# Kernel tuning notes

Measured on AMD Instinct MI355X. Metric: run time of the kernel, lower is better.

Reference implementation:

```python
import jax, jax.numpy as jnp
import numpy as np

N = 50000      # nodes
E = 800000     # edges (avg degree 16)
F_IN = 128     # num_features
H1 = 256       # hidden_dims[0]
H2 = 128       # hidden_dims[1]
D_EMB = 64     # embedding_dim
C_CLS = 2      # num_classes
EPS = 1e-5     # BatchNorm eps


def setup_inputs() -> dict:
    key = jax.random.key(0)
    ks = jax.random.split(key, 24)
    f32 = jnp.float32
    def w(k, shape, scale=0.05):
        return jax.random.normal(k, shape, f32) * scale
    inp = {
        "x": jax.random.normal(ks[0], (N, F_IN), f32),
        "edge_index": jax.random.randint(ks[1], (2, E), 0, N, jnp.int32),
        # input_proj
        "Wp": w(ks[2], (F_IN, H1)), "bp": jnp.zeros((H1,), f32),
        # conv1 (SAGEConv): lin_l (neighbors, with bias), lin_r (root, no bias)
        "W1l": w(ks[3], (F_IN, H1)), "b1l": jnp.zeros((H1,), f32), "W1r": w(ks[4], (F_IN, H1)),
        # bn1 (eval mode, running stats)
        "bn1_g": jnp.ones((H1,), f32), "bn1_b": jnp.zeros((H1,), f32),
        "bn1_m": w(ks[5], (H1,), 0.01), "bn1_v": jnp.ones((H1,), f32) + 0.1 * jax.random.uniform(ks[6], (H1,), f32),
        # skip_proj
        "Wsk": w(ks[7], (H1, H2)), "bsk": jnp.zeros((H2,), f32),
        # conv2
        "W2l": w(ks[8], (H1, H2)), "b2l": jnp.zeros((H2,), f32), "W2r": w(ks[9], (H1, H2)),
        # bn2
        "bn2_g": jnp.ones((H2,), f32), "bn2_b": jnp.zeros((H2,), f32),
        "bn2_m": w(ks[10], (H2,), 0.01), "bn2_v": jnp.ones((H2,), f32) + 0.1 * jax.random.uniform(ks[11], (H2,), f32),
        # conv3
        "W3l": w(ks[12], (H2, D_EMB)), "b3l": jnp.zeros((D_EMB,), f32), "W3r": w(ks[13], (H2, D_EMB)),
        # classifier
        "Wc": w(ks[14], (D_EMB, C_CLS)), "bc": jnp.zeros((C_CLS,), f32),
    }
    return inp


def _sage(h, src, dst, Wl, bl, Wr):
    # mean aggregation of source features into destination nodes
    s = jax.ops.segment_sum(h[src], dst, num_segments=N)        # [N, d]
    cnt = jax.ops.segment_sum(jnp.ones((src.shape[0], 1), h.dtype), dst, num_segments=N)
    mean = s / jnp.maximum(cnt, 1.0)
    return mean @ Wl + bl + h @ Wr


def _bn(h, g, b, m, v):
    return (h - m) * jax.lax.rsqrt(v + EPS) * g + b


def reference(x, edge_index, Wp, bp, W1l, b1l, W1r, bn1_g, bn1_b, bn1_m, bn1_v,
              Wsk, bsk, W2l, b2l, W2r, bn2_g, bn2_b, bn2_m, bn2_v,
              W3l, b3l, W3r, Wc, bc):
    src, dst = edge_index[0], edge_index[1]
    identity = x @ Wp + bp                                # input_proj
    h = _sage(x, src, dst, W1l, b1l, W1r)                 # conv1
    h = jax.nn.relu(_bn(h, bn1_g, bn1_b, bn1_m, bn1_v) + identity)
    # dropout is identity in eval mode
    identity = h @ Wsk + bsk                              # skip_proj
    h = _sage(h, src, dst, W2l, b2l, W2r)                 # conv2
    h = jax.nn.relu(_bn(h, bn2_g, bn2_b, bn2_m, bn2_v) + identity)
    emb = _sage(h, src, dst, W3l, b3l, W3r)               # conv3
    logits = emb @ Wc + bc
    return (logits, emb)
```

## Files before the change

### kernel.cpp

```cpp
#include <hip/hip_runtime.h>
#include <hip/hip_fp16.h>

#define NN 50000
#define NE 800000
#define SLN 6250
#define CAP 64
#define BCAP 106496
constexpr float EPSV = 1e-5f;

typedef __attribute__((ext_vector_type(8))) short short8;
typedef __attribute__((ext_vector_type(4))) float f32x4;

__device__ __forceinline__ float bf2f(unsigned short u) {
    return __uint_as_float(((unsigned int)u) << 16);
}
__device__ __forceinline__ unsigned short f2bf(float f) {
    unsigned int x = __float_as_uint(f);
    return (unsigned short)((x + 0x7FFFu + ((x >> 16) & 1u)) >> 16);
}
__device__ __forceinline__ unsigned char f2e5(float f) {
    unsigned short h = __half_as_ushort(__float2half(f));
    unsigned short r = h + 0x7F + ((h >> 8) & 1);
    return (unsigned char)(r >> 8);
}
__device__ __forceinline__ void acc16(float* a, uint4 u) {
#pragma unroll
    for (int q = 0; q < 4; q++) {
        unsigned int x = (q == 0) ? u.x : (q == 1) ? u.y : (q == 2) ? u.z : u.w;
        unsigned int h01 = ((x << 8) & 0xFF00u) | ((x << 16) & 0xFF000000u);
        unsigned int h23 = ((x >> 8) & 0xFF00u) | (x & 0xFF000000u);
        __half2 p01 = *(__half2*)&h01, p23 = *(__half2*)&h23;
        float2 f01 = __half22float2(p01), f23 = __half22float2(p23);
        a[q * 4 + 0] += f01.x; a[q * 4 + 1] += f01.y;
        a[q * 4 + 2] += f23.x; a[q * 4 + 3] += f23.y;
    }
}

__global__ __launch_bounds__(256) void k_bin(const int* __restrict__ src,
                                             const int* __restrict__ dst,
                                             int* __restrict__ binCnt,
                                             int2* __restrict__ binBuf) {
    __shared__ int hcnt[8];
    __shared__ int hbase[8];
    int tid = threadIdx.x;
    if (tid < 8) hcnt[tid] = 0;
    __syncthreads();
    int q = blockIdx.x * 256 + tid;
    bool val = q < NE / 4;
    int4 d = make_int4(0, 0, 0, 0), s = make_int4(0, 0, 0, 0);
    int b0 = 0, b1 = 0, b2 = 0, b3 = 0, r0 = 0, r1 = 0, r2 = 0, r3 = 0;
    if (val) {
        d = ((const int4*)dst)[q];
        s = ((const int4*)src)[q];
        b0 = d.x / SLN; r0 = atomicAdd(&hcnt[b0], 1);
        b1 = d.y / SLN; r1 = atomicAdd(&hcnt[b1], 1);
        b2 = d.z / SLN; r2 = atomicAdd(&hcnt[b2], 1);
        b3 = d.w / SLN; r3 = atomicAdd(&hcnt[b3], 1);
    }
    __syncthreads();
    if (tid < 8) hbase[tid] = atomicAdd(&binCnt[tid], hcnt[tid]);
    __syncthreads();
    if (val) {
        binBuf[(size_t)b0 * BCAP + hbase[b0] + r0] = make_int2(d.x, s.x);
        binBuf[(size_t)b1 * BCAP + hbase[b1] + r1] = make_int2(d.y, s.y);
        binBuf[(size_t)b2 * BCAP + hbase[b2] + r2] = make_int2(d.z, s.z);
        binBuf[(size_t)b3 * BCAP + hbase[b3] + r3] = make_int2(d.w, s.w);
    }
}

__global__ __launch_bounds__(256) void k_scatter2(const int2* __restrict__ binBuf,
                                                  const int* __restrict__ binCnt,
                                                  int* __restrict__ cnt,
                                                  int* __restrict__ csr) {
    int bin = blockIdx.x & 7;
    int lb = blockIdx.x >> 3;
    int n = binCnt[bin];
    const int2* buf = binBuf + (size_t)bin * BCAP;
    for (int i = lb * 256 + threadIdx.x; i < n; i += 128 * 256) {
        int2 p = buf[i];
        int slot = atomicAdd(&cnt[p.x], 1);
        csr[p.x * CAP + slot] = p.y;
    }
}

__device__ void prep1_body(int t, const float* Wp, const float* bp, const float* W1l,
                           const float* b1l, const float* W1r, const float* g, const float* b,
                           const float* m, const float* v, unsigned short* Wf, float* c) {
    int lane = t & 63, f = (t >> 6) & 3, kt = (t >> 8) & 7;
    int nb = t >> 11;
    int col = nb * 64 + f * 16 + (lane & 15);
    int k0 = kt * 32 + (lane >> 4) * 8;
    float A = g[col] * rsqrtf(v[col] + EPSV);
    unsigned short* o = Wf + (size_t)t * 8;
    for (int j = 0; j < 8; j++) {
        int k = k0 + j;
        float w;
        if (k < 128) w = W1l[k * 256 + col] * A;
        else         w = W1r[(k - 128) * 256 + col] * A + Wp[(k - 128) * 256 + col];
        o[j] = f2bf(w);
    }
    if (t < 256) {
        float At = g[t] * rsqrtf(v[t] + EPSV);
        c[t] = b1l[t] * At + (b[t] - m[t] * At) + bp[t];
    }
}

__device__ void prep2_body(int t, const float* Wsk, const float* bsk, const float* W2l,
                           const float* b2l, const float* W2r, const float* g, const float* b,
                           const float* m, const float* v, unsigned short* Wf, float* c) {
    int lane = t & 63, f = (t >> 6) & 3, kt = (t >> 8) & 7, nb = t >> 11;
    int col = nb * 64 + f * 16 + (lane & 15);
    int k0 = kt * 32 + (lane >> 4) * 8;
    unsigned short* o = Wf + (size_t)t * 8;
    if (col < 128) {
        float A = g[col] * rsqrtf(v[col] + EPSV);
        for (int j = 0; j < 8; j++) o[j] = f2bf(W2l[(k0 + j) * 128 + col] * A);
    } else {
        int cc = col - 128;
        float A = g[cc] * rsqrtf(v[cc] + EPSV);
        for (int j = 0; j < 8; j++)
            o[j] = f2bf(W2r[(k0 + j) * 128 + cc] * A + Wsk[(k0 + j) * 128 + cc]);
    }
    if (t < 128) {
        float At = g[t] * rsqrtf(v[t] + EPSV);
        c[t] = b2l[t] * At + (b[t] - m[t] * At) + bsk[t];
    }
}

__device__ void prep3_body(int t, const float* W3l, const float* b3l, const float* W3r,
                           unsigned short* Wf, float* c) {
    int lane = t & 63, f = (t >> 6) & 3, kt = (t >> 8) & 3, nb = t >> 10;
    int col = nb * 64 + f * 16 + (lane & 15);
    int k0 = kt * 32 + (lane >> 4) * 8;
    unsigned short* o = Wf + (size_t)t * 8;
    if (col < 64) {
        for (int j = 0; j < 8; j++) o[j] = f2bf(W3l[(k0 + j) * 64 + col]);
    } else {
        int cc = col - 64;
        for (int j = 0; j < 8; j++) o[j] = f2bf(W3r[(k0 + j) * 64 + cc]);
    }
    if (t < 64) c[t] = b3l[t];
}

__global__ void k_prep_fused(const float* x, unsigned short* xcat, unsigned char* xf8,
                             int* cnt, int* binCnt,
                             const float* Wp, const float* bp,
                             const float* W1l, const float* b1l, const float* W1r,
                             const float* g1, const float* b1, const float* m1, const float* v1,
                             const float* Wsk, const float* bsk,
                             const float* W2l, const float* b2l, const float* W2r,
                             const float* g2, const float* b2, const float* m2, const float* v2,
                             const float* W3l, const float* b3l, const float* W3r,
                             unsigned short* Wf1, unsigned short* Wf2, unsigned short* Wf3,
                             float* c1, float* c2, float* c3) {
    int bb = blockIdx.x;
    if (bb < 6250) {
        int i = bb * 256 + threadIdx.x;
        if (i < NN / 4) ((int4*)cnt)[i] = make_int4(0, 0, 0, 0);
        if (i < 2) ((int4*)binCnt)[i] = make_int4(0, 0, 0, 0);
        if (i >= NN * 128 / 4) return;
        int r = i >> 5, c4 = (i & 31) * 4;
        float4 v = ((const float4*)x)[i];
        ushort4 u = make_ushort4(f2bf(v.x), f2bf(v.y), f2bf(v.z), f2bf(v.w));
        *(ushort4*)&xcat[(size_t)r * 256 + 128 + c4] = u;
        uchar4 u8 = make_uchar4(f2e5(v.x), f2e5(v.y), f2e5(v.z), f2e5(v.w));
        *(uchar4*)&xf8[(size_t)r * 128 + c4] = u8;
    } else if (bb < 6282) {
        prep1_body((bb - 6250) * 256 + threadIdx.x, Wp, bp, W1l, b1l, W1r, g1, b1, m1, v1, Wf1, c1);
    } else if (bb < 6314) {
        prep2_body((bb - 6282) * 256 + threadIdx.x, Wsk, bsk, W2l, b2l, W2r, g2, b2, m2, v2, Wf2, c2);
    } else {
        prep3_body((bb - 6314) * 256 + threadIdx.x, W3l, b3l, W3r, Wf3, c3);
    }
}

__global__ __launch_bounds__(256) void k_gemm12(const unsigned short* __restrict__ xcat,
                                                const unsigned short* __restrict__ Wf1,
                                                const float* __restrict__ c1,
                                                const unsigned short* __restrict__ Wf2,
                                                unsigned short* __restrict__ r2,
                                                unsigned char* __restrict__ pf8) {
    constexpr int KT = 8;
    constexpr int HS = 268;
    __shared__ unsigned short Bs[256 * 32];
    __shared__ unsigned short hs[64 * HS];
    int tid = threadIdx.x;
    int lane = tid & 63, w = tid >> 6;
    int bm = blockIdx.x;
    int rbase = bm * 64 + w * 16;

    int ra = rbase + (lane & 15);
    if (ra >= NN) ra = NN - 1;
    const unsigned short* ap = xcat + (size_t)ra * 256 + ((lane >> 4) * 8);
    short8 afr[KT];
#pragma unroll
    for (int kt = 0; kt < KT; kt++) afr[kt] = *(const short8*)(ap + kt * 32);

    int skt = tid >> 5;
    int sj = (tid & 31) * 4;
    float4* bsd = (float4*)Bs + skt * 128 + sj;

    auto csrc = [&](int c) -> const float4* {
        const unsigned short* W = (c < 8) ? Wf1 : Wf2;
        int nb = (c & 7) >> 1, sub = c & 1;
        return (const float4*)W + (size_t)nb * 2048 + skt * 256 + sub * 128 + sj;
    };
    float4 pre0, pre1, pre2, pre3;
    { const float4* s = csrc(0); pre0 = s[0]; pre1 = s[1]; pre2 = s[2]; pre3 = s[3]; }

    int hrow0 = w * 16 + (lane >> 4) * 4;

    for (int nb = 0; nb < 4; nb++) {
        f32x4 acc[4];
#pragma unroll
        for (int f = 0; f < 4; f++) acc[f] = (f32x4){0.f, 0.f, 0.f, 0.f};
#pragma unroll
        for (int sub = 0; sub < 2; sub++) {
            int c = nb * 2 + sub;
            __syncthreads();
            bsd[0] = pre0; bsd[1] = pre1; bsd[2] = pre2; bsd[3] = pre3;
            __syncthreads();
            { const float4* s = csrc(c + 1); pre0 = s[0]; pre1 = s[1]; pre2 = s[2]; pre3 = s[3]; }
#pragma unroll
            for (int kt = 0; kt < KT; kt++) {
#pragma unroll
                for (int fr = 0; fr < 2; fr++) {
                    short8 bfr = *(const short8*)&Bs[((kt * 2 + fr) * 64 + lane) * 8];
                    acc[sub * 2 + fr] = __builtin_amdgcn_mfma_f32_16x16x32_bf16(afr[kt], bfr, acc[sub * 2 + fr], 0, 0, 0);
                }
            }
        }
        int cc = nb * 64 + (lane & 15);
#pragma unroll
        for (int f = 0; f < 4; f++) {
            int col = cc + f * 16;
            float bv = c1[col];
#pragma unroll
            for (int r = 0; r < 4; r++) {
                float val = fmaxf(acc[f][r] + bv, 0.f);
                hs[(hrow0 + r) * HS + col] = f2bf(val);
            }
        }
    }

    short8 a2[KT];
    {
        const unsigned short* hp = &hs[(w * 16 + (lane & 15)) * HS + ((lane >> 4) * 8)];
#pragma unroll
        for (int kt = 0; kt < KT; kt++) a2[kt] = *(const short8*)(hp + kt * 32);
    }

    int gr0 = rbase + (lane >> 4) * 4;
    for (int nb = 0; nb < 4; nb++) {
        f32x4 acc[4];
#pragma unroll
        for (int f = 0; f < 4; f++) acc[f] = (f32x4){0.f, 0.f, 0.f, 0.f};
#pragma unroll
        for (int sub = 0; sub < 2; sub++) {
            int c = 8 + nb * 2 + sub;
            __syncthreads();
            bsd[0] = pre0; bsd[1] = pre1; bsd[2] = pre2; bsd[3] = pre3;
            __syncthreads();
            if (c < 15) { const float4* s = csrc(c + 1); pre0 = s[0]; pre1 = s[1]; pre2 = s[2]; pre3 = s[3]; }
#pragma unroll
            for (int kt = 0; kt < KT; kt++) {
#pragma unroll
                for (int fr = 0; fr < 2; fr++) {
                    short8 bfr = *(const short8*)&Bs[((kt * 2 + fr) * 64 + lane) * 8];
                    acc[sub * 2 + fr] = __builtin_amdgcn_mfma_f32_16x16x32_bf16(a2[kt], bfr, acc[sub * 2 + fr], 0, 0, 0);
                }
            }
        }
        int cc = nb * 64 + (lane & 15);
#pragma unroll
        for (int f = 0; f < 4; f++) {
            int col = cc + f * 16;
#pragma unroll
            for (int r = 0; r < 4; r++) {
                int gr = gr0 + r;
                if (gr < NN) {
                    float val = acc[f][r];
                    if (col < 128) pf8[(size_t)gr * 128 + col] = f2e5(val);
                    else           r2[(size_t)gr * 128 + (col - 128)] = f2bf(val);
                }
            }
        }
    }
}

__global__ __launch_bounds__(256) void k_gemm3(const unsigned short* __restrict__ h2,
                                               const unsigned short* __restrict__ Wf3,
                                               unsigned short* __restrict__ G3) {
    constexpr int KT = 4;
    __shared__ unsigned short Bs[128 * 64];
    int tid = threadIdx.x;
    int lane = tid & 63, w = tid >> 6;
    int bm = blockIdx.x;

    int ra = bm * 64 + w * 16 + (lane & 15);
    if (ra >= NN) ra = NN - 1;
    const unsigned short* ap = h2 + (size_t)ra * 128 + ((lane >> 4) * 8);
    short8 afr[KT];
#pragma unroll
    for (int kt = 0; kt < KT; kt++) afr[kt] = *(const short8*)(ap + kt * 32);

    int gr0 = bm * 64 + w * 16 + (lane >> 4) * 4;

    for (int nb = 0; nb < 2; nb++) {
        __syncthreads();
        {
            const float4* srcp = (const float4*)(Wf3 + (size_t)nb * 128 * 64);
            float4* dsts = (float4*)Bs;
            for (int i = tid; i < 128 * 8; i += 256) dsts[i] = srcp[i];
        }
        __syncthreads();
        f32x4 acc[4];
#pragma unroll
        for (int f = 0; f < 4; f++) acc[f] = (f32x4){0.f, 0.f, 0.f, 0.f};
#pragma unroll
        for (int kt = 0; kt < KT; kt++) {
#pragma unroll
            for (int f = 0; f < 4; f++) {
                short8 bfr = *(const short8*)&Bs[((kt * 4 + f) * 64 + lane) * 8];
                acc[f] = __builtin_amdgcn_mfma_f32_16x16x32_bf16(afr[kt], bfr, acc[f], 0, 0, 0);
            }
        }
        int cc = nb * 64 + (lane & 15);
#pragma unroll
        for (int f = 0; f < 4; f++) {
#pragma unroll
            for (int r = 0; r < 4; r++) {
                int gr = gr0 + r;
                if (gr < NN) G3[(size_t)gr * 128 + cc + f * 16] = f2bf(acc[f][r]);
            }
        }
    }
}


__global__ __launch_bounds__(256) void k_aggx(const int* __restrict__ cnt,
                                              const int* __restrict__ csr,
                                              const unsigned char* __restrict__ xf8,
                                              unsigned short* __restrict__ xcat) {
    int lane = threadIdx.x & 63, wv = threadIdx.x >> 6;
    int node = blockIdx.x * 4 + wv;
    int deg = cnt[node];
    const int* cp = csr + node * CAP;
    int g = lane >> 3, l8 = lane & 7;
    float a[16];
#pragma unroll
    for (int j = 0; j < 16; j++) a[j] = 0.f;
    const unsigned char* base = xf8 + l8 * 16;
    int e = 0;
    for (; e + 16 <= deg; e += 16) {
        int s0 = cp[e + g], s1 = cp[e + 8 + g];
        uint4 u0 = *(const uint4*)(base + (size_t)s0 * 128);
        uint4 u1 = *(const uint4*)(base + (size_t)s1 * 128);
        acc16(a, u0); acc16(a, u1);
    }
    if (e + g < deg) {
        uint4 u = *(const uint4*)(base + (size_t)cp[e + g] * 128);
        acc16(a, u);
    }
    if (e + 8 + g < deg) {
        uint4 u = *(const uint4*)(base + (size_t)cp[e + 8 + g] * 128);
        acc16(a, u);
    }
#pragma unroll
    for (int j = 0; j < 16; j++) {
        a[j] += __shfl_xor(a[j], 8);
        a[j] += __shfl_xor(a[j], 16);
        a[j] += __shfl_xor(a[j], 32);
    }
    if (lane < 8) {
        float inv = 1.f / (float)max(deg, 1);
        unsigned short o[16];
#pragma unroll
        for (int j = 0; j < 16; j++) o[j] = f2bf(a[j] * inv);
        *(short8*)&xcat[(size_t)node * 256 + lane * 16] = *(short8*)&o[0];
        *(short8*)&xcat[(size_t)node * 256 + lane * 16 + 8] = *(short8*)&o[8];
    }
}

__global__ __launch_bounds__(256) void k_agg2(const unsigned char* __restrict__ pf8,
                                              const unsigned short* __restrict__ r2,
                                              const int* __restrict__ cnt,
                                              const int* __restrict__ csr,
                                              const float* __restrict__ c,
                                              unsigned short* __restrict__ h2) {
    int lane = threadIdx.x & 63, wv = threadIdx.x >> 6;
    int node = blockIdx.x * 4 + wv;
    int deg = cnt[node];
    const int* cp = csr + node * CAP;
    int g = lane >> 3, l8 = lane & 7;
    float a[16];
#pragma unroll
    for (int j = 0; j < 16; j++) a[j] = 0.f;
    const unsigned char* base = pf8 + l8 * 16;
    int e = 0;
    for (; e + 16 <= deg; e += 16) {
        int s0 = cp[e + g], s1 = cp[e + 8 + g];
        uint4 u0 = *(const uint4*)(base + (size_t)s0 * 128);
        uint4 u1 = *(const uint4*)(base + (size_t)s1 * 128);
        acc16(a, u0); acc16(a, u1);
    }
    if (e + g < deg) {
        uint4 u = *(const uint4*)(base + (size_t)cp[e + g] * 128);
        acc16(a, u);
    }
    if (e + 8 + g < deg) {
        uint4 u = *(const uint4*)(base + (size_t)cp[e + 8 + g] * 128);
        acc16(a, u);
    }
#pragma unroll
    for (int j = 0; j < 16; j++) {
        a[j] += __shfl_xor(a[j], 8);
        a[j] += __shfl_xor(a[j], 16);
        a[j] += __shfl_xor(a[j], 32);
    }
    if (lane < 8) {
        float inv = 1.f / (float)max(deg, 1);
        short8 rA = *(const short8*)&r2[(size_t)node * 128 + lane * 16];
        short8 rB = *(const short8*)&r2[(size_t)node * 128 + lane * 16 + 8];
        const float* cpb = c + lane * 16;
        unsigned short o[16];
#pragma unroll
        for (int j = 0; j < 8; j++)
            o[j] = f2bf(fmaxf(a[j] * inv + bf2f(rA[j]) + cpb[j], 0.f));
#pragma unroll
        for (int j = 0; j < 8; j++)
            o[8 + j] = f2bf(fmaxf(a[8 + j] * inv + bf2f(rB[j]) + cpb[8 + j], 0.f));
        *(short8*)&h2[(size_t)node * 128 + lane * 16] = *(short8*)&o[0];
        *(short8*)&h2[(size_t)node * 128 + lane * 16 + 8] = *(short8*)&o[8];
    }
}

__global__ __launch_bounds__(256) void k_agg_final(const unsigned short* __restrict__ G,
                                                   const int* __restrict__ cnt,
                                                   const int* __restrict__ csr,
                                                   const float* __restrict__ c,
                                                   const float* __restrict__ Wc,
                                                   const float* __restrict__ bc,
                                                   float* __restrict__ outbuf) {
    int lane = threadIdx.x & 63, wv = threadIdx.x >> 6;
    int node = blockIdx.x * 4 + wv;
    int deg = cnt[node];
    const int* cp = csr + node * CAP;
    int g = lane >> 3, l8 = lane & 7;
    float a[8];
#pragma unroll
    for (int j = 0; j < 8; j++) a[j] = 0.f;
    const unsigned short* base = G + l8 * 8;
    int e = 0;
    for (; e + 32 <= deg; e += 32) {
        int s0 = cp[e + g], s1 = cp[e + 8 + g], s2 = cp[e + 16 + g], s3 = cp[e + 24 + g];
        short8 u0 = *(const short8*)(base + (size_t)s0 * 128);
        short8 u1 = *(const short8*)(base + (size_t)s1 * 128);
        short8 u2 = *(const short8*)(base + (size_t)s2 * 128);
        short8 u3 = *(const short8*)(base + (size_t)s3 * 128);
#pragma unroll
        for (int j = 0; j < 8; j++)
            a[j] += (bf2f(u0[j]) + bf2f(u1[j])) + (bf2f(u2[j]) + bf2f(u3[j]));
    }
    for (; e + 8 <= deg; e += 8) {
        short8 u = *(const short8*)(base + (size_t)cp[e + g] * 128);
#pragma unroll
        for (int j = 0; j < 8; j++) a[j] += bf2f(u[j]);
    }
    if (e + g < deg) {
        short8 u = *(const short8*)(base + (size_t)cp[e + g] * 128);
#pragma unroll
        for (int j = 0; j < 8; j++) a[j] += bf2f(u[j]);
    }
#pragma unroll
    for (int j = 0; j < 8; j++) {
        a[j] += __shfl_xor(a[j], 8);
        a[j] += __shfl_xor(a[j], 16);
        a[j] += __shfl_xor(a[j], 32);
    }
    float l0 = 0.f, l1 = 0.f;
    if (lane < 8) {
        float inv = 1.f / (float)max(deg, 1);
        short8 r = *(const short8*)&G[(size_t)node * 128 + 64 + l8 * 8];
        const float* cpb = c + l8 * 8;
        float v[8];
#pragma unroll
        for (int j = 0; j < 8; j++) v[j] = a[j] * inv + bf2f(r[j]) + cpb[j];
        float* emb = outbuf + 2 * (size_t)NN;
        *(float4*)&emb[(size_t)node * 64 + l8 * 8] = make_float4(v[0], v[1], v[2], v[3]);
        *(float4*)&emb[(size_t)node * 64 + l8 * 8 + 4] = make_float4(v[4], v[5], v[6], v[7]);
        int c0 = l8 * 8;
#pragma unroll
        for (int j = 0; j < 8; j++) {
            l0 += v[j] * Wc[2 * (c0 + j)];
            l1 += v[j] * Wc[2 * (c0 + j) + 1];
        }
    }
    l0 += __shfl_xor(l0, 1); l1 += __shfl_xor(l1, 1);
    l0 += __shfl_xor(l0, 2); l1 += __shfl_xor(l1, 2);
    l0 += __shfl_xor(l0, 4); l1 += __shfl_xor(l1, 4);
    if (lane == 0) {
        outbuf[(size_t)node * 2 + 0] = l0 + bc[0];
        outbuf[(size_t)node * 2 + 1] = l1 + bc[1];
    }
}

extern "C" void kernel_launch(void* const* d_in, const int* in_sizes, int n_in,
                              void* d_out, int out_size, void* d_ws, size_t ws_size,
                              hipStream_t stream) {
    const float* x    = (const float*)d_in[0];
    const int*   ei   = (const int*)d_in[1];
    const float* Wp   = (const float*)d_in[2];
    const float* bp   = (const float*)d_in[3];
    const float* W1l  = (const float*)d_in[4];
    const float* b1l  = (const float*)d_in[5];
    const float* W1r  = (const float*)d_in[6];
    const float* bn1g = (const float*)d_in[7];
    const float* bn1b = (const float*)d_in[8];
    const float* bn1m = (const float*)d_in[9];
    const float* bn1v = (const float*)d_in[10];
    const float* Wsk  = (const float*)d_in[11];
    const float* bsk  = (const float*)d_in[12];
    const float* W2l  = (const float*)d_in[13];
    const float* b2l  = (const float*)d_in[14];
    const float* W2r  = (const float*)d_in[15];
    const float* bn2g = (const float*)d_in[16];
    const float* bn2b = (const float*)d_in[17];
    const float* bn2m = (const float*)d_in[18];
    const float* bn2v = (const float*)d_in[19];
    const float* W3l  = (const float*)d_in[20];
    const float* b3l  = (const float*)d_in[21];
    const float* W3r  = (const float*)d_in[22];
    const float* Wc   = (const float*)d_in[23];
    const float* bc   = (const float*)d_in[24];

    const int* src = ei;
    const int* dst = ei + NE;

    char* ws = (char*)d_ws;
    size_t o = 0;
    auto alloc = [&](size_t b) -> char* {
        char* p = ws + o;
        o = (o + b + 255) & ~(size_t)255;
        return p;
    };
    int* cnt    = (int*)alloc((size_t)NN * 4);
    int* binCnt = (int*)alloc(64);
    int* csr    = (int*)alloc((size_t)NN * CAP * 4);
    unsigned char*  xf8  = (unsigned char*)alloc((size_t)NN * 128);
    unsigned short* xcat = (unsigned short*)alloc((size_t)NN * 256 * 2);
    unsigned char*  pf8  = (unsigned char*)alloc((size_t)NN * 128);
    unsigned short* r2   = (unsigned short*)alloc((size_t)NN * 128 * 2);
    unsigned short* h2   = (unsigned short*)alloc((size_t)NN * 128 * 2);
    unsigned short* G3   = (unsigned short*)alloc((size_t)NN * 128 * 2);
    unsigned short* Wf1  = (unsigned short*)alloc((size_t)256 * 256 * 2);
    unsigned short* Wf2  = (unsigned short*)alloc((size_t)256 * 256 * 2);
    unsigned short* Wf3  = (unsigned short*)alloc((size_t)128 * 128 * 2);
    float* c1 = (float*)alloc(256 * 4);
    float* c2 = (float*)alloc(128 * 4);
    float* c3 = (float*)alloc(64 * 4);
    int2* binBuf = (int2*)G3;

    float* outbuf = (float*)d_out;

    k_prep_fused<<<6322, 256, 0, stream>>>(x, xcat, xf8, cnt, binCnt,
                                           Wp, bp, W1l, b1l, W1r, bn1g, bn1b, bn1m, bn1v,
                                           Wsk, bsk, W2l, b2l, W2r, bn2g, bn2b, bn2m, bn2v,
                                           W3l, b3l, W3r, Wf1, Wf2, Wf3, c1, c2, c3);

    k_bin<<<782, 256, 0, stream>>>(src, dst, binCnt, binBuf);
    k_scatter2<<<1024, 256, 0, stream>>>(binBuf, binCnt, cnt, csr);

    k_aggx<<<12500, 256, 0, stream>>>(cnt, csr, xf8, xcat);

    k_gemm12<<<782, 256, 0, stream>>>(xcat, Wf1, c1, Wf2, r2, pf8);
    k_agg2<<<12500, 256, 0, stream>>>(pf8, r2, cnt, csr, c2, h2);

    k_gemm3<<<782, 256, 0, stream>>>(h2, Wf3, G3);
    k_agg_final<<<12500, 256, 0, stream>>>(G3, cnt, csr, c3, Wc, bc, outbuf);
}
```

Before: 202.9 us.

## Double-buffer weight tiles in fused GEMM12 with one barrier per chunk

The fused two-layer GEMM now stages weight tiles in smaller 16-column chunks held in two LDS buffers. The next chunk is prefetched into registers and written to the alternate buffer while the current chunk feeds MFMA, so each chunk needs one barrier instead of two. The aim is to shorten barrier stalls and overlap global weight loads with compute. In exchange there are twice as many chunks, a single accumulator chain per chunk that limits MFMA interleaving, and a fully unrolled two-phase loop that may raise code size and register pressure.

```diff
diff --git a/kernel.cpp b/kernel.cpp
--- a/kernel.cpp
+++ b/kernel.cpp
@@ -182,7 +182,7 @@
                                                 unsigned char* __restrict__ pf8) {
     constexpr int KT = 8;
     constexpr int HS = 268;
-    __shared__ unsigned short Bs[256 * 32];
+    __shared__ unsigned short Bs[2][256 * 16];
     __shared__ unsigned short hs[64 * HS];
     int tid = threadIdx.x;
     int lane = tid & 63, w = tid >> 6;
@@ -196,92 +196,85 @@
 #pragma unroll
     for (int kt = 0; kt < KT; kt++) afr[kt] = *(const short8*)(ap + kt * 32);
 
-    int skt = tid >> 5;
-    int sj = (tid & 31) * 4;
-    float4* bsd = (float4*)Bs + skt * 128 + sj;
-
     auto csrc = [&](int c) -> const float4* {
-        const unsigned short* W = (c < 8) ? Wf1 : Wf2;
-        int nb = (c & 7) >> 1, sub = c & 1;
-        return (const float4*)W + (size_t)nb * 2048 + skt * 256 + sub * 128 + sj;
+        const unsigned short* W = (c < 16) ? Wf1 : Wf2;
+        int q = c & 15;
+        return (const float4*)W + (size_t)(q >> 2) * 2048 + (q & 3) * 64;
     };
-    float4 pre0, pre1, pre2, pre3;
-    { const float4* s = csrc(0); pre0 = s[0]; pre1 = s[1]; pre2 = s[2]; pre3 = s[3]; }
+    int si0 = (tid >> 6) * 256 + (tid & 63);
+    int si1 = ((tid + 256) >> 6) * 256 + (tid & 63);
+
+    {
+        const float4* s = csrc(0);
+        float4* d = (float4*)Bs[0];
+        d[tid] = s[si0];
+        d[tid + 256] = s[si1];
+    }
+    __syncthreads();
 
     int hrow0 = w * 16 + (lane >> 4) * 4;
-
-    for (int nb = 0; nb < 4; nb++) {
-        f32x4 acc[4];
-#pragma unroll
-        for (int f = 0; f < 4; f++) acc[f] = (f32x4){0.f, 0.f, 0.f, 0.f};
-#pragma unroll
-        for (int sub = 0; sub < 2; sub++) {
-            int c = nb * 2 + sub;
-            __syncthreads();
-            bsd[0] = pre0; bsd[1] = pre1; bsd[2] = pre2; bsd[3] = pre3;
-            __syncthreads();
-            { const float4* s = csrc(c + 1); pre0 = s[0]; pre1 = s[1]; pre2 = s[2]; pre3 = s[3]; }
-#pragma unroll
-            for (int kt = 0; kt < KT; kt++) {
-#pragma unroll
-                for (int fr = 0; fr < 2; fr++) {
-                    short8 bfr = *(const short8*)&Bs[((kt * 2 + fr) * 64 + lane) * 8];
-                    acc[sub * 2 + fr] = __builtin_amdgcn_mfma_f32_16x16x32_bf16(afr[kt], bfr, acc[sub * 2 + fr], 0, 0, 0);
+    int gr0 = rbase + (lane >> 4) * 4;
+    short8 a2[KT];
+    float4 pre0, pre1;
+    f32x4 acc[4];
+
+#pragma unroll
+    for (int ph = 0; ph < 2; ph++) {
+        if (ph == 1) {
+            const unsigned short* hp = &hs[(w * 16 + (lane & 15)) * HS + ((lane >> 4) * 8)];
+#pragma unroll
+            for (int kt = 0; kt < KT; kt++) a2[kt] = *(const short8*)(hp + kt * 32);
+        }
+#pragma unroll
+        for (int nb = 0; nb < 4; nb++) {
+#pragma unroll
+            for (int f = 0; f < 4; f++) {
+                const int c = ph * 16 + nb * 4 + f;
+                if (c < 31) {
+                    const float4* s = csrc(c + 1);
+                    pre0 = s[si0];
+                    pre1 = s[si1];
                 }
+                const unsigned short* bsp = Bs[c & 1];
+                f32x4 a = (f32x4){0.f, 0.f, 0.f, 0.f};
+#pragma unroll
+                for (int kt = 0; kt < KT; kt++) {
+                    short8 bfr = *(const short8*)&bsp[(kt * 64 + lane) * 8];
+                    a = __builtin_amdgcn_mfma_f32_16x16x32_bf16(ph == 0 ? afr[kt] : a2[kt], bfr, a, 0, 0, 0);
+                }
+                acc[f] = a;
+                if (c < 31) {
+                    float4* d = (float4*)Bs[(c + 1) & 1];
+                    d[tid] = pre0;
+                    d[tid + 256] = pre1;
+                }
+                __syncthreads();
             }
-        }
-        int cc = nb * 64 + (lane & 15);
-#pragma unroll
-        for (int f = 0; f < 4; f++) {
-            int col = cc + f * 16;
-            float bv = c1[col];
-#pragma unroll
-            for (int r = 0; r < 4; r++) {
-                float val = fmaxf(acc[f][r] + bv, 0.f);
-                hs[(hrow0 + r) * HS + col] = f2bf(val);
-            }
-        }
-    }
-
-    short8 a2[KT];
-    {
-        const unsigned short* hp = &hs[(w * 16 + (lane & 15)) * HS + ((lane >> 4) * 8)];
-#pragma unroll
-        for (int kt = 0; kt < KT; kt++) a2[kt] = *(const short8*)(hp + kt * 32);
-    }
-
-    int gr0 = rbase + (lane >> 4) * 4;
-    for (int nb = 0; nb < 4; nb++) {
-        f32x4 acc[4];
-#pragma unroll
-        for (int f = 0; f < 4; f++) acc[f] = (f32x4){0.f, 0.f, 0.f, 0.f};
-#pragma unroll
-        for (int sub = 0; sub < 2; sub++) {
-            int c = 8 + nb * 2 + sub;
-            __syncthreads();
-            bsd[0] = pre0; bsd[1] = pre1; bsd[2] = pre2; bsd[3] = pre3;
-            __syncthreads();
-            if (c < 15) { const float4* s = csrc(c + 1); pre0 = s[0]; pre1 = s[1]; pre2 = s[2]; pre3 = s[3]; }
-#pragma unroll
-            for (int kt = 0; kt < KT; kt++) {
-#pragma unroll
-                for (int fr = 0; fr < 2; fr++) {
-                    short8 bfr = *(const short8*)&Bs[((kt * 2 + fr) * 64 + lane) * 8];
-                    acc[sub * 2 + fr] = __builtin_amdgcn_mfma_f32_16x16x32_bf16(a2[kt], bfr, acc[sub * 2 + fr], 0, 0, 0);
+            int cc = nb * 64 + (lane & 15);
+            if (ph == 0) {
+#pragma unroll
+                for (int f = 0; f < 4; f++) {
+                    int col = cc + f * 16;
+                    float bv = c1[col];
+#pragma unroll
+                    for (int r = 0; r < 4; r++) {
+                        float val = fmaxf(acc[f][r] + bv, 0.f);
+                        hs[(hrow0 + r) * HS + col] = f2bf(val);
+                    }
                 }
-            }
-        }
-        int cc = nb * 64 + (lane & 15);
-#pragma unroll
-        for (int f = 0; f < 4; f++) {
-            int col = cc + f * 16;
-#pragma unroll
-            for (int r = 0; r < 4; r++) {
-                int gr = gr0 + r;
-                if (gr < NN) {
-                    float val = acc[f][r];
-                    if (col < 128) pf8[(size_t)gr * 128 + col] = f2e5(val);
-                    else           r2[(size_t)gr * 128 + (col - 128)] = f2bf(val);
+            } else {
+#pragma unroll
+                for (int f = 0; f < 4; f++) {
+                    int col = cc + f * 16;
+#pragma unroll
+                    for (int r = 0; r < 4; r++) {
+                        int gr = gr0 + r;
+                        if (gr < NN) {
+                            float val = acc[f][r];
+                            if (col < 128) pf8[(size_t)gr * 128 + col] = f2e5(val);
+                            else           r2[(size_t)gr * 128 + (col - 128)] = f2bf(val);
+                        }
+                    }
                 }
             }
         }
```

Result: no change. 201.1 us (-0.9%).

## Load GEMM weight fragments directly from global memory instead of staging in LDS

Applied to the files above, without the earlier changes.

The two GEMM kernels stop staging weight tiles through shared memory with double-buffered prefetch and __syncthreads barriers. Each wave now reads its pre-swizzled bf16 B fragments straight from global memory, which the L2/L1 caches serve since the weights are small and shared by all blocks. This drops the per-chunk barriers and LDS traffic and frees LDS for occupancy. In exchange every wave issues its own redundant global loads, and MFMA issue may stall on cache latency with no explicit prefetch.

```diff
diff --git a/kernel.cpp b/kernel.cpp
--- a/kernel.cpp
+++ b/kernel.cpp
@@ -182,7 +182,6 @@
                                                 unsigned char* __restrict__ pf8) {
     constexpr int KT = 8;
     constexpr int HS = 268;
-    __shared__ unsigned short Bs[256 * 32];
     __shared__ unsigned short hs[64 * HS];
     int tid = threadIdx.x;
     int lane = tid & 63, w = tid >> 6;
@@ -196,52 +195,43 @@
 #pragma unroll
     for (int kt = 0; kt < KT; kt++) afr[kt] = *(const short8*)(ap + kt * 32);
 
-    int skt = tid >> 5;
-    int sj = (tid & 31) * 4;
-    float4* bsd = (float4*)Bs + skt * 128 + sj;
-
-    auto csrc = [&](int c) -> const float4* {
-        const unsigned short* W = (c < 8) ? Wf1 : Wf2;
-        int nb = (c & 7) >> 1, sub = c & 1;
-        return (const float4*)W + (size_t)nb * 2048 + skt * 256 + sub * 128 + sj;
-    };
-    float4 pre0, pre1, pre2, pre3;
-    { const float4* s = csrc(0); pre0 = s[0]; pre1 = s[1]; pre2 = s[2]; pre3 = s[3]; }
+    const short8* bf1 = (const short8*)Wf1 + lane;
+    const short8* bf2 = (const short8*)Wf2 + lane;
 
     int hrow0 = w * 16 + (lane >> 4) * 4;
-
+    int gr0 = rbase + (lane >> 4) * 4;
+
+#pragma unroll
     for (int nb = 0; nb < 4; nb++) {
-        f32x4 acc[4];
-#pragma unroll
-        for (int f = 0; f < 4; f++) acc[f] = (f32x4){0.f, 0.f, 0.f, 0.f};
-#pragma unroll
-        for (int sub = 0; sub < 2; sub++) {
-            int c = nb * 2 + sub;
-            __syncthreads();
-            bsd[0] = pre0; bsd[1] = pre1; bsd[2] = pre2; bsd[3] = pre3;
-            __syncthreads();
-            { const float4* s = csrc(c + 1); pre0 = s[0]; pre1 = s[1]; pre2 = s[2]; pre3 = s[3]; }
-#pragma unroll
-            for (int kt = 0; kt < KT; kt++) {
-#pragma unroll
-                for (int fr = 0; fr < 2; fr++) {
-                    short8 bfr = *(const short8*)&Bs[((kt * 2 + fr) * 64 + lane) * 8];
-                    acc[sub * 2 + fr] = __builtin_amdgcn_mfma_f32_16x16x32_bf16(afr[kt], bfr, acc[sub * 2 + fr], 0, 0, 0);
-                }
-            }
+        f32x4 acc0 = (f32x4){0.f, 0.f, 0.f, 0.f};
+        f32x4 acc1 = acc0, acc2 = acc0, acc3 = acc0;
+#pragma unroll
+        for (int kt = 0; kt < KT; kt++) {
+            const short8* bb = bf1 + nb * 2048 + kt * 256;
+            short8 b0 = bb[0];
+            short8 b1 = bb[64];
+            short8 b2 = bb[128];
+            short8 b3 = bb[192];
+            acc0 = __builtin_amdgcn_mfma_f32_16x16x32_bf16(afr[kt], b0, acc0, 0, 0, 0);
+            acc1 = __builtin_amdgcn_mfma_f32_16x16x32_bf16(afr[kt], b1, acc1, 0, 0, 0);
+            acc2 = __builtin_amdgcn_mfma_f32_16x16x32_bf16(afr[kt], b2, acc2, 0, 0, 0);
+            acc3 = __builtin_amdgcn_mfma_f32_16x16x32_bf16(afr[kt], b3, acc3, 0, 0, 0);
         }
         int cc = nb * 64 + (lane & 15);
+        f32x4 av[4] = {acc0, acc1, acc2, acc3};
 #pragma unroll
         for (int f = 0; f < 4; f++) {
             int col = cc + f * 16;
             float bv = c1[col];
 #pragma unroll
             for (int r = 0; r < 4; r++) {
-                float val = fmaxf(acc[f][r] + bv, 0.f);
+                float val = fmaxf(av[f][r] + bv, 0.f);
                 hs[(hrow0 + r) * HS + col] = f2bf(val);
             }
         }
     }
+
+    __syncthreads();
 
     short8 a2[KT];
     {
@@ -250,28 +240,24 @@
         for (int kt = 0; kt < KT; kt++) a2[kt] = *(const short8*)(hp + kt * 32);
     }
 
-    int gr0 = rbase + (lane >> 4) * 4;
+#pragma unroll
     for (int nb = 0; nb < 4; nb++) {
-        f32x4 acc[4];
-#pragma unroll
-        for (int f = 0; f < 4; f++) acc[f] = (f32x4){0.f, 0.f, 0.f, 0.f};
-#pragma unroll
-        for (int sub = 0; sub < 2; sub++) {
-            int c = 8 + nb * 2 + sub;
-            __syncthreads();
-            bsd[0] = pre0; bsd[1] = pre1; bsd[2] = pre2; bsd[3] = pre3;
-            __syncthreads();
-            if (c < 15) { const float4* s = csrc(c + 1); pre0 = s[0]; pre1 = s[1]; pre2 = s[2]; pre3 = s[3]; }
-#pragma unroll
-            for (int kt = 0; kt < KT; kt++) {
-#pragma unroll
-                for (int fr = 0; fr < 2; fr++) {
-                    short8 bfr = *(const short8*)&Bs[((kt * 2 + fr) * 64 + lane) * 8];
-                    acc[sub * 2 + fr] = __builtin_amdgcn_mfma_f32_16x16x32_bf16(a2[kt], bfr, acc[sub * 2 + fr], 0, 0, 0);
-                }
-            }
+        f32x4 acc0 = (f32x4){0.f, 0.f, 0.f, 0.f};
+        f32x4 acc1 = acc0, acc2 = acc0, acc3 = acc0;
+#pragma unroll
+        for (int kt = 0; kt < KT; kt++) {
+            const short8* bb = bf2 + nb * 2048 + kt * 256;
+            short8 b0 = bb[0];
+            short8 b1 = bb[64];
+            short8 b2 = bb[128];
+            short8 b3 = bb[192];
+            acc0 = __builtin_amdgcn_mfma_f32_16x16x32_bf16(a2[kt], b0, acc0, 0, 0, 0);
+            acc1 = __builtin_amdgcn_mfma_f32_16x16x32_bf16(a2[kt], b1, acc1, 0, 0, 0);
+            acc2 = __builtin_amdgcn_mfma_f32_16x16x32_bf16(a2[kt], b2, acc2, 0, 0, 0);
+            acc3 = __builtin_amdgcn_mfma_f32_16x16x32_bf16(a2[kt], b3, acc3, 0, 0, 0);
         }
         int cc = nb * 64 + (lane & 15);
+        f32x4 av[4] = {acc0, acc1, acc2, acc3};
 #pragma unroll
         for (int f = 0; f < 4; f++) {
             int col = cc + f * 16;
@@ -279,7 +265,7 @@
             for (int r = 0; r < 4; r++) {
                 int gr = gr0 + r;
                 if (gr < NN) {
-                    float val = acc[f][r];
+                    float val = av[f][r];
                     if (col < 128) pf8[(size_t)gr * 128 + col] = f2e5(val);
                     else           r2[(size_t)gr * 128 + (col - 128)] = f2bf(val);
                 }
@@ -292,7 +278,6 @@
                                                const unsigned short* __restrict__ Wf3,
                                                unsigned short* __restrict__ G3) {
     constexpr int KT = 4;
-    __shared__ unsigned short Bs[128 * 64];
     int tid = threadIdx.x;
     int lane = tid & 63, w = tid >> 6;
     int bm = blockIdx.x;
@@ -304,34 +289,33 @@
 #pragma unroll
     for (int kt = 0; kt < KT; kt++) afr[kt] = *(const short8*)(ap + kt * 32);
 
+    const short8* bf = (const short8*)Wf3 + lane;
     int gr0 = bm * 64 + w * 16 + (lane >> 4) * 4;
 
+#pragma unroll
     for (int nb = 0; nb < 2; nb++) {
-        __syncthreads();
-        {
-            const float4* srcp = (const float4*)(Wf3 + (size_t)nb * 128 * 64);
-            float4* dsts = (float4*)Bs;
-            for (int i = tid; i < 128 * 8; i += 256) dsts[i] = srcp[i];
-        }
-        __syncthreads();
-        f32x4 acc[4];
-#pragma unroll
-        for (int f = 0; f < 4; f++) acc[f] = (f32x4){0.f, 0.f, 0.f, 0.f};
+        f32x4 acc0 = (f32x4){0.f, 0.f, 0.f, 0.f};
+        f32x4 acc1 = acc0, acc2 = acc0, acc3 = acc0;
 #pragma unroll
         for (int kt = 0; kt < KT; kt++) {
-#pragma unroll
-            for (int f = 0; f < 4; f++) {
-                short8 bfr = *(const short8*)&Bs[((kt * 4 + f) * 64 + lane) * 8];
-                acc[f] = __builtin_amdgcn_mfma_f32_16x16x32_bf16(afr[kt], bfr, acc[f], 0, 0, 0);
-            }
+            const short8* bb = bf + nb * 1024 + kt * 256;
+            short8 b0 = bb[0];
+            short8 b1 = bb[64];
+            short8 b2 = bb[128];
+            short8 b3 = bb[192];
+            acc0 = __builtin_amdgcn_mfma_f32_16x16x32_bf16(afr[kt], b0, acc0, 0, 0, 0);
+            acc1 = __builtin_amdgcn_mfma_f32_16x16x32_bf16(afr[kt], b1, acc1, 0, 0, 0);
+            acc2 = __builtin_amdgcn_mfma_f32_16x16x32_bf16(afr[kt], b2, acc2, 0, 0, 0);
+            acc3 = __builtin_amdgcn_mfma_f32_16x16x32_bf16(afr[kt], b3, acc3, 0, 0, 0);
         }
         int cc = nb * 64 + (lane & 15);
+        f32x4 av[4] = {acc0, acc1, acc2, acc3};
 #pragma unroll
         for (int f = 0; f < 4; f++) {
 #pragma unroll
             for (int r = 0; r < 4; r++) {
                 int gr = gr0 + r;
-                if (gr < NN) G3[(size_t)gr * 128 + cc + f * 16] = f2bf(acc[f][r]);
+                if (gr < NN) G3[(size_t)gr * 128 + cc + f * 16] = f2bf(av[f][r]);
             }
         }
     }
```

Measured after the change: 203.4 us. No clear change (+0.3%).

## Fuse edge binning into prep kernel and stage full weight tiles in gemm12

Applied to the files above, without the earlier changes.

The edge-binning kernel becomes extra blocks of the fused prep kernel, and the bin counters are zeroed by a memset placed before it. This removes one launch and lets binning overlap with the feature conversion. Separately, gemm12 now stages a whole 256x64 weight tile in shared memory per output block, replacing the register-prefetched double-half staging. That halves the barrier count but drops the prefetch overlap and doubles shared memory, which may lower occupancy.

```diff
diff --git a/kernel.cpp b/kernel.cpp
--- a/kernel.cpp
+++ b/kernel.cpp
@@ -33,38 +33,6 @@
         float2 f01 = __half22float2(p01), f23 = __half22float2(p23);
         a[q * 4 + 0] += f01.x; a[q * 4 + 1] += f01.y;
         a[q * 4 + 2] += f23.x; a[q * 4 + 3] += f23.y;
-    }
-}
-
-__global__ __launch_bounds__(256) void k_bin(const int* __restrict__ src,
-                                             const int* __restrict__ dst,
-                                             int* __restrict__ binCnt,
-                                             int2* __restrict__ binBuf) {
-    __shared__ int hcnt[8];
-    __shared__ int hbase[8];
-    int tid = threadIdx.x;
-    if (tid < 8) hcnt[tid] = 0;
-    __syncthreads();
-    int q = blockIdx.x * 256 + tid;
-    bool val = q < NE / 4;
-    int4 d = make_int4(0, 0, 0, 0), s = make_int4(0, 0, 0, 0);
-    int b0 = 0, b1 = 0, b2 = 0, b3 = 0, r0 = 0, r1 = 0, r2 = 0, r3 = 0;
-    if (val) {
-        d = ((const int4*)dst)[q];
-        s = ((const int4*)src)[q];
-        b0 = d.x / SLN; r0 = atomicAdd(&hcnt[b0], 1);
-        b1 = d.y / SLN; r1 = atomicAdd(&hcnt[b1], 1);
-        b2 = d.z / SLN; r2 = atomicAdd(&hcnt[b2], 1);
-        b3 = d.w / SLN; r3 = atomicAdd(&hcnt[b3], 1);
-    }
-    __syncthreads();
-    if (tid < 8) hbase[tid] = atomicAdd(&binCnt[tid], hcnt[tid]);
-    __syncthreads();
-    if (val) {
-        binBuf[(size_t)b0 * BCAP + hbase[b0] + r0] = make_int2(d.x, s.x);
-        binBuf[(size_t)b1 * BCAP + hbase[b1] + r1] = make_int2(d.y, s.y);
-        binBuf[(size_t)b2 * BCAP + hbase[b2] + r2] = make_int2(d.z, s.z);
-        binBuf[(size_t)b3 * BCAP + hbase[b3] + r3] = make_int2(d.w, s.w);
     }
 }
 
@@ -144,6 +112,7 @@
 
 __global__ void k_prep_fused(const float* x, unsigned short* xcat, unsigned char* xf8,
                              int* cnt, int* binCnt,
+                             const int* src, const int* dst, int2* binBuf,
                              const float* Wp, const float* bp,
                              const float* W1l, const float* b1l, const float* W1r,
                              const float* g1, const float* b1, const float* m1, const float* v1,
@@ -153,11 +122,13 @@
                              const float* W3l, const float* b3l, const float* W3r,
                              unsigned short* Wf1, unsigned short* Wf2, unsigned short* Wf3,
                              float* c1, float* c2, float* c3) {
+    __shared__ int hcnt[8];
+    __shared__ int hbase[8];
     int bb = blockIdx.x;
+    int tid = threadIdx.x;
     if (bb < 6250) {
-        int i = bb * 256 + threadIdx.x;
+        int i = bb * 256 + tid;
         if (i < NN / 4) ((int4*)cnt)[i] = make_int4(0, 0, 0, 0);
-        if (i < 2) ((int4*)binCnt)[i] = make_int4(0, 0, 0, 0);
         if (i >= NN * 128 / 4) return;
         int r = i >> 5, c4 = (i & 31) * 4;
         float4 v = ((const float4*)x)[i];
@@ -166,11 +137,35 @@
         uchar4 u8 = make_uchar4(f2e5(v.x), f2e5(v.y), f2e5(v.z), f2e5(v.w));
         *(uchar4*)&xf8[(size_t)r * 128 + c4] = u8;
     } else if (bb < 6282) {
-        prep1_body((bb - 6250) * 256 + threadIdx.x, Wp, bp, W1l, b1l, W1r, g1, b1, m1, v1, Wf1, c1);
+        prep1_body((bb - 6250) * 256 + tid, Wp, bp, W1l, b1l, W1r, g1, b1, m1, v1, Wf1, c1);
     } else if (bb < 6314) {
-        prep2_body((bb - 6282) * 256 + threadIdx.x, Wsk, bsk, W2l, b2l, W2r, g2, b2, m2, v2, Wf2, c2);
+        prep2_body((bb - 6282) * 256 + tid, Wsk, bsk, W2l, b2l, W2r, g2, b2, m2, v2, Wf2, c2);
+    } else if (bb < 6322) {
+        prep3_body((bb - 6314) * 256 + tid, W3l, b3l, W3r, Wf3, c3);
     } else {
-        prep3_body((bb - 6314) * 256 + threadIdx.x, W3l, b3l, W3r, Wf3, c3);
+        if (tid < 8) hcnt[tid] = 0;
+        __syncthreads();
+        int q = (bb - 6322) * 256 + tid;
+        bool val = q < NE / 4;
+        int4 d = make_int4(0, 0, 0, 0), s = make_int4(0, 0, 0, 0);
+        int b0 = 0, b1i = 0, b2i = 0, b3i = 0, r0 = 0, r1 = 0, r2 = 0, r3 = 0;
+        if (val) {
+            d = ((const int4*)dst)[q];
+            s = ((const int4*)src)[q];
+            b0 = d.x / SLN; r0 = atomicAdd(&hcnt[b0], 1);
+            b1i = d.y / SLN; r1 = atomicAdd(&hcnt[b1i], 1);
+            b2i = d.z / SLN; r2 = atomicAdd(&hcnt[b2i], 1);
+            b3i = d.w / SLN; r3 = atomicAdd(&hcnt[b3i], 1);
+        }
+        __syncthreads();
+        if (tid < 8) hbase[tid] = atomicAdd(&binCnt[tid], hcnt[tid]);
+        __syncthreads();
+        if (val) {
+            binBuf[(size_t)b0 * BCAP + hbase[b0] + r0] = make_int2(d.x, s.x);
+            binBuf[(size_t)b1i * BCAP + hbase[b1i] + r1] = make_int2(d.y, s.y);
+            binBuf[(size_t)b2i * BCAP + hbase[b2i] + r2] = make_int2(d.z, s.z);
+            binBuf[(size_t)b3i * BCAP + hbase[b3i] + r3] = make_int2(d.w, s.w);
+        }
     }
 }
 
@@ -181,8 +176,8 @@
                                                 unsigned short* __restrict__ r2,
                                                 unsigned char* __restrict__ pf8) {
     constexpr int KT = 8;
-    constexpr int HS = 268;
-    __shared__ unsigned short Bs[256 * 32];
+    constexpr int HS = 272;
+    __shared__ unsigned short Bs[256 * 64];
     __shared__ unsigned short hs[64 * HS];
     int tid = threadIdx.x;
     int lane = tid & 63, w = tid >> 6;
@@ -196,38 +191,25 @@
 #pragma unroll
     for (int kt = 0; kt < KT; kt++) afr[kt] = *(const short8*)(ap + kt * 32);
 
-    int skt = tid >> 5;
-    int sj = (tid & 31) * 4;
-    float4* bsd = (float4*)Bs + skt * 128 + sj;
-
-    auto csrc = [&](int c) -> const float4* {
-        const unsigned short* W = (c < 8) ? Wf1 : Wf2;
-        int nb = (c & 7) >> 1, sub = c & 1;
-        return (const float4*)W + (size_t)nb * 2048 + skt * 256 + sub * 128 + sj;
-    };
-    float4 pre0, pre1, pre2, pre3;
-    { const float4* s = csrc(0); pre0 = s[0]; pre1 = s[1]; pre2 = s[2]; pre3 = s[3]; }
-
     int hrow0 = w * 16 + (lane >> 4) * 4;
 
     for (int nb = 0; nb < 4; nb++) {
+        __syncthreads();
+        {
+            const float4* srcp = (const float4*)(Wf1 + (size_t)nb * 256 * 64);
+            float4* dsts = (float4*)Bs;
+            for (int i = tid; i < 256 * 8; i += 256) dsts[i] = srcp[i];
+        }
+        __syncthreads();
         f32x4 acc[4];
 #pragma unroll
         for (int f = 0; f < 4; f++) acc[f] = (f32x4){0.f, 0.f, 0.f, 0.f};
 #pragma unroll
-        for (int sub = 0; sub < 2; sub++) {
-            int c = nb * 2 + sub;
-            __syncthreads();
-            bsd[0] = pre0; bsd[1] = pre1; bsd[2] = pre2; bsd[3] = pre3;
-            __syncthreads();
-            { const float4* s = csrc(c + 1); pre0 = s[0]; pre1 = s[1]; pre2 = s[2]; pre3 = s[3]; }
-#pragma unroll
-            for (int kt = 0; kt < KT; kt++) {
-#pragma unroll
-                for (int fr = 0; fr < 2; fr++) {
-                    short8 bfr = *(const short8*)&Bs[((kt * 2 + fr) * 64 + lane) * 8];
-                    acc[sub * 2 + fr] = __builtin_amdgcn_mfma_f32_16x16x32_bf16(afr[kt], bfr, acc[sub * 2 + fr], 0, 0, 0);
-                }
+        for (int kt = 0; kt < KT; kt++) {
+#pragma unroll
+            for (int f = 0; f < 4; f++) {
+                short8 bfr = *(const short8*)&Bs[((kt * 4 + f) * 64 + lane) * 8];
+                acc[f] = __builtin_amdgcn_mfma_f32_16x16x32_bf16(afr[kt], bfr, acc[f], 0, 0, 0);
             }
         }
         int cc = nb * 64 + (lane & 15);
@@ -252,23 +234,22 @@
 
     int gr0 = rbase + (lane >> 4) * 4;
     for (int nb = 0; nb < 4; nb++) {
+        __syncthreads();
+        {
+            const float4* srcp = (const float4*)(Wf2 + (size_t)nb * 256 * 64);
+            float4* dsts = (float4*)Bs;
+            for (int i = tid; i < 256 * 8; i += 256) dsts[i] = srcp[i];
+        }
+        __syncthreads();
         f32x4 acc[4];
 #pragma unroll
         for (int f = 0; f < 4; f++) acc[f] = (f32x4){0.f, 0.f, 0.f, 0.f};
 #pragma unroll
-        for (int sub = 0; sub < 2; sub++) {
-            int c = 8 + nb * 2 + sub;
-            __syncthreads();
-            bsd[0] = pre0; bsd[1] = pre1; bsd[2] = pre2; bsd[3] = pre3;
-            __syncthreads();
-            if (c < 15) { const float4* s = csrc(c + 1); pre0 = s[0]; pre1 = s[1]; pre2 = s[2]; pre3 = s[3]; }
-#pragma unroll
-            for (int kt = 0; kt < KT; kt++) {
-#pragma unroll
-                for (int fr = 0; fr < 2; fr++) {
-                    short8 bfr = *(const short8*)&Bs[((kt * 2 + fr) * 64 + lane) * 8];
-                    acc[sub * 2 + fr] = __builtin_amdgcn_mfma_f32_16x16x32_bf16(a2[kt], bfr, acc[sub * 2 + fr], 0, 0, 0);
-                }
+        for (int kt = 0; kt < KT; kt++) {
+#pragma unroll
+            for (int f = 0; f < 4; f++) {
+                short8 bfr = *(const short8*)&Bs[((kt * 4 + f) * 64 + lane) * 8];
+                acc[f] = __builtin_amdgcn_mfma_f32_16x16x32_bf16(a2[kt], bfr, acc[f], 0, 0, 0);
             }
         }
         int cc = nb * 64 + (lane & 15);
@@ -563,12 +544,12 @@
 
     float* outbuf = (float*)d_out;
 
-    k_prep_fused<<<6322, 256, 0, stream>>>(x, xcat, xf8, cnt, binCnt,
+    hipMemsetAsync(binCnt, 0, 64, stream);
+    k_prep_fused<<<7104, 256, 0, stream>>>(x, xcat, xf8, cnt, binCnt, src, dst, binBuf,
                                            Wp, bp, W1l, b1l, W1r, bn1g, bn1b, bn1m, bn1v,
                                            Wsk, bsk, W2l, b2l, W2r, bn2g, bn2b, bn2m, bn2v,
                                            W3l, b3l, W3r, Wf1, Wf2, Wf3, c1, c2, c3);
 
-    k_bin<<<782, 256, 0, stream>>>(src, dst, binCnt, binBuf);
     k_scatter2<<<1024, 256, 0, stream>>>(binBuf, binCnt, cnt, csr);
 
     k_aggx<<<12500, 256, 0, stream>>>(cnt, csr, xf8, xcat);
```

New measurement: 201.8 us. No clear change (-0.5%).
